# Performance work log

Measured on AMD Instinct MI355X. Metric: run time of the kernel, lower is better.

Reference implementation:

```python
import jax, jax.numpy as jnp
import numpy as np

VOCAB = 50257
BATCH = 512
SEQ = 1024


def setup_inputs() -> dict:
    key = jax.random.key(0)
    kx, kidf = jax.random.split(key)
    x = jax.random.randint(kx, (BATCH, SEQ), 0, VOCAB, dtype=jnp.int64)
    # idf weights are positive; uniform in (0.1, 5.0) mimics real idf values
    idf = jax.random.uniform(kidf, (VOCAB,), dtype=jnp.float32, minval=0.1, maxval=5.0)
    return {"x": x, "idf": idf}


def reference(x, idf):
    B, S = x.shape
    V = idf.shape[0]
    # term-frequency histogram: scatter-add directly into (B, V) accumulator,
    # equivalent to the one-hot scatter_ + sum over seq in the original
    rows = jnp.arange(B, dtype=x.dtype)[:, None]           # (B, 1)
    tf = jnp.zeros((B, V), dtype=jnp.float32).at[rows, x].add(1.0)
    tfidf = tf * idf                                        # (B, V)
    n = jnp.sum(tfidf, axis=1, keepdims=True)               # (B, 1)
    return tfidf / n
```

## Files before the change

kernel.cpp:

```cpp
#include <hip/hip_runtime.h>


constexpr int VOCAB   = 50257;
constexpr int SEQ     = 1024;
constexpr int BATCH   = 512;
constexpr int HWORDS  = (VOCAB + 1) / 2;
constexpr int HWORDS4 = ((HWORDS + 3) / 4) * 4;
constexpr int NT      = 1024;
constexpr int NGROUP  = VOCAB >> 2;

struct __attribute__((packed)) f4p { float4 v; };

__global__ __launch_bounds__(NT)
void tfidf_kernel(const int* __restrict__ x,
                  const float* __restrict__ idf,
                  float* __restrict__ out) {
    __shared__ __align__(16) unsigned int cnt[HWORDS4];
    __shared__ float red[NT / 64];

    const int b   = blockIdx.x;
    const int tid = threadIdx.x;

    const int tok = x[(size_t)b * SEQ + tid];

    {
        uint4* z = (uint4*)cnt;
        const uint4 z4 = make_uint4(0u, 0u, 0u, 0u);
        for (int i = tid; i < HWORDS4 / 4; i += NT) z[i] = z4;
    }

    const float my_idf = idf[tok];
    __syncthreads();

    atomicAdd(&cnt[tok >> 1], (tok & 1) ? 65536u : 1u);

    float v = my_idf;
    #pragma unroll
    for (int off = 32; off > 0; off >>= 1) v += __shfl_down(v, off, 64);
    if ((tid & 63) == 0) red[tid >> 6] = v;
    __syncthreads();
    float nsum = 0.0f;
    #pragma unroll
    for (int w = 0; w < NT / 64; ++w) nsum += red[w];
    const float inv_n = 1.0f / nsum;

    float* __restrict__ orow = out + (size_t)b * VOCAB;
    const float4* __restrict__ idf4 = (const float4*)idf;
    f4p* __restrict__ o4 = (f4p*)orow;

    for (int c = tid; c < NGROUP; c += NT) {
        const uint2  w = *(const uint2*)&cnt[2 * c];
        const float4 f = idf4[c];
        float4 r;
        r.x = (float)(w.x & 0xffffu) * f.x * inv_n;
        r.y = (float)(w.x >> 16)     * f.y * inv_n;
        r.z = (float)(w.y & 0xffffu) * f.z * inv_n;
        r.w = (float)(w.y >> 16)     * f.w * inv_n;
        o4[c].v = r;
    }
    if (tid == 0) {
        orow[VOCAB - 1] =
            (float)(cnt[(VOCAB - 1) >> 1] & 0xffffu) * idf[VOCAB - 1] * inv_n;
    }
}

extern "C" void kernel_launch(void* const* d_in, const int* in_sizes, int n_in,
                              void* d_out, int out_size, void* d_ws, size_t ws_size,
                              hipStream_t stream) {
    const int*   x   = (const int*)d_in[0];
    const float* idf = (const float*)d_in[1];
    float*       out = (float*)d_out;
    tfidf_kernel<<<dim3(BATCH), dim3(NT), 0, stream>>>(x, idf, out);
}
```

Measured before the change: 110.6 us.

## Split each row's vocabulary into two halves handled by separate blocks

Launches two blocks per batch row, each owning half the vocabulary. Each block keeps a smaller shared-memory histogram, counts only the tokens that fall in its half, and writes only its half of the output. This cuts LDS use per block so more blocks can be resident at once, which should help hide memory latency. The cost is that every block still reads all tokens and idf values to compute the full normalizer, so that work is now done twice.

```diff
diff --git a/kernel.cpp b/kernel.cpp
--- a/kernel.cpp
+++ b/kernel.cpp
@@ -1,38 +1,47 @@
 #include <hip/hip_runtime.h>
 
 
-constexpr int VOCAB   = 50257;
-constexpr int SEQ     = 1024;
-constexpr int BATCH   = 512;
-constexpr int HWORDS  = (VOCAB + 1) / 2;
-constexpr int HWORDS4 = ((HWORDS + 3) / 4) * 4;
-constexpr int NT      = 1024;
-constexpr int NGROUP  = VOCAB >> 2;
+constexpr int VOCAB  = 50257;
+constexpr int SEQ    = 1024;
+constexpr int BATCH  = 512;
+constexpr int NT     = 1024;
+constexpr int SEGV   = (VOCAB + 1) / 2;
+constexpr int SWORDS = (SEGV + 1) / 2;
+constexpr int SWORDS4 = ((SWORDS + 3) / 4) * 4;
 
 struct __attribute__((packed)) f4p { float4 v; };
 
-__global__ __launch_bounds__(NT)
+__global__ __launch_bounds__(NT, 8)
 void tfidf_kernel(const int* __restrict__ x,
                   const float* __restrict__ idf,
                   float* __restrict__ out) {
-    __shared__ __align__(16) unsigned int cnt[HWORDS4];
+    __shared__ __align__(16) unsigned int cnt[SWORDS4];
     __shared__ float red[NT / 64];
 
-    const int b   = blockIdx.x;
+    const int blk = blockIdx.x;
+    const int b   = blk >> 1;
+    const int s   = blk & 1;
     const int tid = threadIdx.x;
+
+    const int lo  = s * SEGV;
+    const int len = s ? (VOCAB - SEGV) : SEGV;
 
     const int tok = x[(size_t)b * SEQ + tid];
 
     {
         uint4* z = (uint4*)cnt;
         const uint4 z4 = make_uint4(0u, 0u, 0u, 0u);
-        for (int i = tid; i < HWORDS4 / 4; i += NT) z[i] = z4;
+        for (int i = tid; i < SWORDS4 / 4; i += NT) z[i] = z4;
     }
 
     const float my_idf = idf[tok];
     __syncthreads();
 
-    atomicAdd(&cnt[tok >> 1], (tok & 1) ? 65536u : 1u);
+    {
+        const unsigned t = (unsigned)(tok - lo);
+        if (t < (unsigned)len)
+            atomicAdd(&cnt[t >> 1], (t & 1) ? 65536u : 1u);
+    }
 
     float v = my_idf;
     #pragma unroll
@@ -44,13 +53,14 @@
     for (int w = 0; w < NT / 64; ++w) nsum += red[w];
     const float inv_n = 1.0f / nsum;
 
-    float* __restrict__ orow = out + (size_t)b * VOCAB;
-    const float4* __restrict__ idf4 = (const float4*)idf;
+    float* __restrict__ orow = out + (size_t)b * VOCAB + lo;
+    const f4p* __restrict__ idf4 = (const f4p*)(idf + lo);
     f4p* __restrict__ o4 = (f4p*)orow;
+    const int n4 = len >> 2;
 
-    for (int c = tid; c < NGROUP; c += NT) {
+    for (int c = tid; c < n4; c += NT) {
         const uint2  w = *(const uint2*)&cnt[2 * c];
-        const float4 f = idf4[c];
+        const float4 f = idf4[c].v;
         float4 r;
         r.x = (float)(w.x & 0xffffu) * f.x * inv_n;
         r.y = (float)(w.x >> 16)     * f.y * inv_n;
@@ -58,9 +68,9 @@
         r.w = (float)(w.y >> 16)     * f.w * inv_n;
         o4[c].v = r;
     }
-    if (tid == 0) {
-        orow[VOCAB - 1] =
-            (float)(cnt[(VOCAB - 1) >> 1] & 0xffffu) * idf[VOCAB - 1] * inv_n;
+    if (tid == 0 && (len & 3)) {
+        const int i = n4 << 2;
+        orow[i] = (float)(cnt[i >> 1] & 0xffffu) * idf[lo + i] * inv_n;
     }
 }
 
@@ -70,5 +80,5 @@
     const int*   x   = (const int*)d_in[0];
     const float* idf = (const float*)d_in[1];
     float*       out = (float*)d_out;
-    tfidf_kernel<<<dim3(BATCH), dim3(NT), 0, stream>>>(x, idf, out);
+    tfidf_kernel<<<dim3(BATCH * 2), dim3(NT), 0, stream>>>(x, idf, out);
 }
```

After: 112.9 us. +2.1%, slower.
